# Kernel tuning notes

Measured on AMD Instinct MI355X. Metric: run time of the kernel, lower is better.

Reference implementation:

```python
import jax, jax.numpy as jnp
import numpy as np
from jax import lax

IN_FEATURES = 1024
NUM_TAGS = 128
C = NUM_TAGS + 3          # CRF adds start/stop (+1 pad slot per original code)
START_IDX = C - 2
STOP_IDX = C - 1
NEG = -10000.0


def setup_inputs() -> dict:
    key = jax.random.key(0)
    k1, k2, k3, k4 = jax.random.split(key, 4)
    B, L = 64, 512
    x = jax.random.normal(k1, (B, L, IN_FEATURES), dtype=jnp.float32)
    mask = jnp.ones((B, L), dtype=jnp.float32)
    W = jax.random.normal(k2, (C, IN_FEATURES), dtype=jnp.float32) * (1.0 / np.sqrt(IN_FEATURES))
    b = jax.random.normal(k3, (C,), dtype=jnp.float32) * 0.01
    transitions = jax.random.normal(k4, (C, C), dtype=jnp.float32)
    # transitions[i, j] = score of transitioning FROM j TO i
    transitions = transitions.at[START_IDX, :].set(NEG)   # never transition into start
    transitions = transitions.at[:, STOP_IDX].set(NEG)    # never transition out of stop
    return {"x": x, "mask": mask, "W": W, "b": b, "transitions": transitions}


def reference(x, mask, W, b, transitions):
    """CRF forward: linear projection + Viterbi decode.
    Returns (best_score [B], best_paths [B, L])."""
    feats = jnp.einsum("bld,cd->blc", x, W) + b          # [B, L, C]
    B, L, Cn = feats.shape

    init_score = jnp.full((B, Cn), NEG, dtype=feats.dtype).at[:, START_IDX].set(0.0)

    def viterbi_step(score, inp):
        feat_t, mask_t = inp                              # [B, C], [B]
        # acc[b, i, j] = score[b, j] + transitions[i, j]
        acc = score[:, None, :] + transitions[None, :, :]  # [B, C, C]
        best = jnp.max(acc, axis=-1)                      # [B, C]
        bp = jnp.argmax(acc, axis=-1).astype(jnp.int32)   # [B, C]
        m = mask_t[:, None]
        new_score = (best + feat_t) * m + score * (1.0 - m)
        return new_score, bp

    final_score, bps = lax.scan(
        viterbi_step, init_score,
        (jnp.transpose(feats, (1, 0, 2)), mask.T))        # bps: [L, B, C]

    final_score = final_score + transitions[STOP_IDX]     # [B, C]
    best_score = jnp.max(final_score, axis=-1)            # [B]
    best_tag = jnp.argmax(final_score, axis=-1).astype(jnp.int32)  # [B]

    def backtrack(tag, bp_t):
        # tag: current tag at timestep t; bp_t: [B, C] backpointers at t
        prev = jnp.take_along_axis(bp_t, tag[:, None], axis=1)[:, 0]
        return prev, tag                                  # emit tag at timestep t

    _, path = lax.scan(backtrack, best_tag, bps, reverse=True)  # path: [L, B]
    best_paths = path.T                                   # [B, L]
    return best_score, best_paths
```

## Files before the change

### kernel.cpp

```cpp
#include <hip/hip_runtime.h>

#define BB 64
#define LL 512
#define DD 1024
#define CC 131
#define CP 132
#define START_I 129
#define STOP_I 130
#define NEGV -10000.0f

__device__ __forceinline__ void lds_barrier() {
    asm volatile("s_waitcnt lgkmcnt(0)" ::: "memory");
    __builtin_amdgcn_s_barrier();
    __builtin_amdgcn_sched_barrier(0);
}

#define GM 64
#define GK 32
#define LSTR 36

__global__ __launch_bounds__(256, 2) void gemm_feats(
    const float* __restrict__ x, const float* __restrict__ W,
    const float* __restrict__ bias, float* __restrict__ feats)
{
    __shared__ float xs[GM * LSTR];
    __shared__ float ws[CP * LSTR];

    const int tid = threadIdx.x;
    const int m0 = blockIdx.x * GM;
    const int tm = tid & 15;
    const int tj = (tid >> 4) & 15;
    const bool tail = (tj < 3);
    const int tjt = (tj < 3) ? tj : 2;

    float acc[4][8];
    float acct[4];
#pragma unroll
    for (int r = 0; r < 4; ++r) {
        acct[r] = 0.f;
#pragma unroll
        for (int c = 0; c < 8; ++c) acc[r][c] = 0.f;
    }

    for (int kc = 0; kc < DD / GK; ++kc) {
        const int k0 = kc * GK;
        if (kc) __syncthreads();
#pragma unroll
        for (int q = 0; q < 2; ++q) {
            int lin = tid + q * 256;
            int m = lin >> 3, c4 = lin & 7;
            float4 v = *(const float4*)&x[(size_t)(m0 + m) * DD + k0 + c4 * 4];
            *(float4*)&xs[m * LSTR + c4 * 4] = v;
        }
#pragma unroll
        for (int q = 0; q < 5; ++q) {
            int lin = tid + q * 256;
            if (lin < CC * 8) {
                int r = lin >> 3, c4 = lin & 7;
                float4 v = *(const float4*)&W[(size_t)r * DD + k0 + c4 * 4];
                *(float4*)&ws[r * LSTR + c4 * 4] = v;
            }
        }
        __syncthreads();

#pragma unroll
        for (int k4 = 0; k4 < 8; ++k4) {
            float4 xr[4], wr[8], wt;
#pragma unroll
            for (int r = 0; r < 4; ++r)
                xr[r] = *(const float4*)&xs[(tm + 16 * r) * LSTR + k4 * 4];
#pragma unroll
            for (int c = 0; c < 8; ++c)
                wr[c] = *(const float4*)&ws[(tj + 16 * c) * LSTR + k4 * 4];
            wt = *(const float4*)&ws[(128 + tjt) * LSTR + k4 * 4];
#pragma unroll
            for (int r = 0; r < 4; ++r) {
#pragma unroll
                for (int c = 0; c < 8; ++c) {
                    acc[r][c] = fmaf(xr[r].x, wr[c].x, acc[r][c]);
                    acc[r][c] = fmaf(xr[r].y, wr[c].y, acc[r][c]);
                    acc[r][c] = fmaf(xr[r].z, wr[c].z, acc[r][c]);
                    acc[r][c] = fmaf(xr[r].w, wr[c].w, acc[r][c]);
                }
                acct[r] = fmaf(xr[r].x, wt.x, acct[r]);
                acct[r] = fmaf(xr[r].y, wt.y, acct[r]);
                acct[r] = fmaf(xr[r].z, wt.z, acct[r]);
                acct[r] = fmaf(xr[r].w, wt.w, acct[r]);
            }
        }
    }

#pragma unroll
    for (int c = 0; c < 8; ++c) {
        int j = tj + 16 * c;
        float bv = bias[j];
#pragma unroll
        for (int r = 0; r < 4; ++r)
            feats[(size_t)(m0 + tm + 16 * r) * CP + j] = acc[r][c] + bv;
    }
    if (tail) {
        int j = 128 + tj;
        float bv = bias[j];
#pragma unroll
        for (int r = 0; r < 4; ++r)
            feats[(size_t)(m0 + tm + 16 * r) * CP + j] = acct[r] + bv;
    }
}

__global__ __launch_bounds__(512, 1) void viterbi_fwd(
    const float* __restrict__ feats, const float* __restrict__ mask,
    const float* __restrict__ trans, float* __restrict__ hist)
{
    const int b = blockIdx.x;
    const int tid = threadIdx.x;
    const int w = tid >> 6, lane = tid & 63;

    __shared__ float sbuf[2][144];
    __shared__ float pbuf[7][132];

    const float* fb = feats + (size_t)b * LL * CP;
    const float* mb = mask + (size_t)b * LL;
    float* hb = hist + (size_t)b * LL * CP;

    int sub, trow = 0;
    bool twr = false;
    float4 TA[5], TB[5];
    if (w < 7) {
        sub = w;
        const int i0 = sub * 20;
        const float* trA = trans + (size_t)lane * CC;
        const float* trB = trans + (size_t)(64 + lane) * CC;
#pragma unroll
        for (int q = 0; q < 5; ++q) {
            int i = i0 + 4 * q;
            TA[q].x = (i + 0 < CC) ? trA[i + 0] : NEGV;
            TA[q].y = (i + 1 < CC) ? trA[i + 1] : NEGV;
            TA[q].z = (i + 2 < CC) ? trA[i + 2] : NEGV;
            TA[q].w = (i + 3 < CC) ? trA[i + 3] : NEGV;
            TB[q].x = (i + 0 < CC) ? trB[i + 0] : NEGV;
            TB[q].y = (i + 1 < CC) ? trB[i + 1] : NEGV;
            TB[q].z = (i + 2 < CC) ? trB[i + 2] : NEGV;
            TB[q].w = (i + 3 < CC) ? trB[i + 3] : NEGV;
        }
    } else {
        const int ln = (lane < 21) ? lane : 20;
        const int s7 = ln / 3;
        const int r3 = ln - s7 * 3;
        sub = s7;
        trow = 128 + r3;
        twr = (lane < 21);
        const int i0 = sub * 20;
        const float* tr = trans + (size_t)trow * CC;
#pragma unroll
        for (int q = 0; q < 5; ++q) {
            int i = i0 + 4 * q;
            TA[q].x = (i + 0 < CC) ? tr[i + 0] : NEGV;
            TA[q].y = (i + 1 < CC) ? tr[i + 1] : NEGV;
            TA[q].z = (i + 2 < CC) ? tr[i + 2] : NEGV;
            TA[q].w = (i + 3 < CC) ? tr[i + 3] : NEGV;
        }
    }

    for (int q = tid; q < 2 * 144; q += 512) {
        int bi = q / 144, idx = q - bi * 144;
        sbuf[bi][idx] = (bi == 0 && idx == START_I) ? 0.f : NEGV;
    }
    __syncthreads();

    const int k = tid;
    const bool cl = (tid < 131);
    float s_prev = (k == START_I) ? 0.f : NEGV;
    float fv0 = 0.f, fv1 = 0.f, mv0 = 1.f, mv1 = 1.f;
    if (cl) { fv0 = fb[k]; fv1 = fb[CP + k]; mv0 = mb[0]; mv1 = mb[1]; }
    const float* fb_t = fb + 2 * CP + k;
    const float* mb_t = mb + 2;
    float* hb_t = hb + k;

    for (int t = 0; t < LL; ++t) {
        const int rb = t & 1;

        {
            const float4* s4 = (const float4*)(&sbuf[rb][0]) + sub * 5;
            if (w < 7) {
                float a0 = -3.0e38f, a1 = -3.0e38f, b0 = -3.0e38f, b1 = -3.0e38f;
#pragma unroll
                for (int q = 0; q < 5; ++q) {
                    float4 sv = s4[q];
                    a0 = fmaxf(fmaxf(sv.x + TA[q].x, sv.y + TA[q].y), a0);
                    a1 = fmaxf(fmaxf(sv.z + TA[q].z, sv.w + TA[q].w), a1);
                    b0 = fmaxf(fmaxf(sv.x + TB[q].x, sv.y + TB[q].y), b0);
                    b1 = fmaxf(fmaxf(sv.z + TB[q].z, sv.w + TB[q].w), b1);
                }
                pbuf[sub][lane] = fmaxf(a0, a1);
                pbuf[sub][64 + lane] = fmaxf(b0, b1);
            } else {
                float a0 = -3.0e38f, a1 = -3.0e38f;
#pragma unroll
                for (int q = 0; q < 5; ++q) {
                    float4 sv = s4[q];
                    a0 = fmaxf(fmaxf(sv.x + TA[q].x, sv.y + TA[q].y), a0);
                    a1 = fmaxf(fmaxf(sv.z + TA[q].z, sv.w + TA[q].w), a1);
                }
                if (twr) pbuf[sub][trow] = fmaxf(a0, a1);
            }
        }

        lds_barrier();

        float fv2 = 0.f, mv2 = 1.f;
        if (cl && t + 2 < LL) { fv2 = *fb_t; mv2 = *mb_t; }
        fb_t += CP; ++mb_t;

        if (cl) {
            float p = fmaxf(fmaxf(fmaxf(pbuf[0][k], pbuf[1][k]),
                                  fmaxf(pbuf[2][k], pbuf[3][k])),
                            fmaxf(fmaxf(pbuf[4][k], pbuf[5][k]), pbuf[6][k]));
            float ns = (mv0 != 0.f) ? (p + fv0) : s_prev;
            s_prev = ns;
            sbuf[rb ^ 1][k] = ns;
            *hb_t = ns;
        }
        hb_t += CP;

        lds_barrier();

        fv0 = fv1; fv1 = fv2; mv0 = mv1; mv1 = mv2;
    }
}

__global__ __launch_bounds__(256, 4) void bp_kernel(
    const float* __restrict__ hist, const float* __restrict__ trans,
    unsigned char* __restrict__ bp)
{
    const int b  = blockIdx.x / 5;
    const int jc = blockIdx.x % 5;
    const int tc = blockIdx.y;
    const int tid = threadIdx.x;
    const int j0 = jc * 32;

    __shared__ float Ts[32][136];
    __shared__ float hs[8][132];

    for (int q = 0; q < 17; ++q) {
        int lin = tid + q * 256;
        if (lin < 32 * CC) {
            int r = lin / CC, i = lin - r * CC;
            if (j0 + r < CC) Ts[r][i] = trans[(size_t)(j0 + r) * CC + i];
        }
    }
    {
        const float4* src = (const float4*)(hist + ((size_t)b * LL + tc * 8) * CP);
#pragma unroll
        for (int q = 0; q < 2; ++q) {
            int lin = tid + q * 256;
            if (lin < (8 * CP) / 4) ((float4*)hs)[lin] = src[lin];
        }
    }
    __syncthreads();

    const int jl = tid & 31;
    const int tt = tid >> 5;
    const int j = j0 + jl;
    const int t = tc * 8 + tt + 1;
    if (j >= CC || t >= LL) return;

    float best; int idx;
    {
        float4 tv = *(const float4*)&Ts[jl][128];
        float4 hv = *(const float4*)&hs[tt][128];
        best = hv.z + tv.z; idx = 130;
        float v;
        v = hv.y + tv.y; if (v >= best) { best = v; idx = 129; }
        v = hv.x + tv.x; if (v >= best) { best = v; idx = 128; }
    }
#pragma unroll
    for (int i4 = 31; i4 >= 0; --i4) {
        float4 tv = *(const float4*)&Ts[jl][i4 * 4];
        float4 hv = *(const float4*)&hs[tt][i4 * 4];
        float v;
        v = hv.w + tv.w; if (v >= best) { best = v; idx = i4 * 4 + 3; }
        v = hv.z + tv.z; if (v >= best) { best = v; idx = i4 * 4 + 2; }
        v = hv.y + tv.y; if (v >= best) { best = v; idx = i4 * 4 + 1; }
        v = hv.x + tv.x; if (v >= best) { best = v; idx = i4 * 4 + 0; }
    }
    bp[((size_t)b * LL + t) * CP + j] = (unsigned char)idx;
}

__global__ __launch_bounds__(64, 1) void viterbi_btr(
    const float* __restrict__ hist, const float* __restrict__ trans,
    const unsigned char* __restrict__ bp,
    float* __restrict__ out_score, float* __restrict__ out_path)
{
    const int b = blockIdx.x;
    const int lane = threadIdx.x;
    const float* hb = hist + ((size_t)b * LL + (LL - 1)) * CP;
    const float* ts = trans + (size_t)STOP_I * CC;

    float v0 = hb[lane] + ts[lane];
    float v1 = hb[lane + 64] + ts[lane + 64];
    float v2 = (lane < 3) ? (hb[lane + 128] + ts[lane + 128]) : -3.0e38f;

    float best = v0; int idx = lane;
    if (v1 > best) { best = v1; idx = lane + 64; }
    if (v2 > best) { best = v2; idx = lane + 128; }
#pragma unroll
    for (int off = 32; off >= 1; off >>= 1) {
        float ob = __shfl_xor(best, off, 64);
        int   oi = __shfl_xor(idx, off, 64);
        if (ob > best || (ob == best && oi < idx)) { best = ob; idx = oi; }
    }

    float* op = out_path + (size_t)b * LL;
    if (lane == 0) {
        out_score[b] = best;
        op[LL - 1] = (float)idx;
    }
    int tag = idx;

    __shared__ unsigned char buf[2][1088];
    const unsigned char* bpb = bp + (size_t)b * LL * CP;

    {
        const unsigned int* src = (const unsigned int*)(bpb + (size_t)504 * CP);
        unsigned int* dst = (unsigned int*)buf[1];
#pragma unroll
        for (int q = 0; q < 5; ++q) {
            int lin = lane + q * 64;
            if (lin < 264) dst[lin] = src[lin];
        }
    }
    lds_barrier();

    int cur = 1;
    for (int k = 63; k >= 0; --k) {
        unsigned int r0 = 0, r1 = 0, r2 = 0, r3 = 0, r4 = 0;
        if (k > 0) {
            const unsigned int* src = (const unsigned int*)(bpb + (size_t)(k - 1) * 8 * CP);
            r0 = src[lane];
            r1 = src[lane + 64];
            r2 = src[lane + 128];
            r3 = src[lane + 192];
            if (lane < 8) r4 = src[lane + 256];
        }
        const unsigned char* cb = buf[cur];
#pragma unroll
        for (int s = 7; s >= 0; --s) {
            int t = k * 8 + s;
            if (t >= 1) {
                tag = cb[s * CP + tag];
                if (lane == 0) op[t - 1] = (float)tag;
            }
        }
        if (k > 0) {
            unsigned int* dst = (unsigned int*)buf[cur ^ 1];
            dst[lane] = r0;
            dst[lane + 64] = r1;
            dst[lane + 128] = r2;
            dst[lane + 192] = r3;
            if (lane < 8) dst[lane + 256] = r4;
            lds_barrier();
        }
        cur ^= 1;
    }
}

extern "C" void kernel_launch(void* const* d_in, const int* in_sizes, int n_in,
                              void* d_out, int out_size, void* d_ws, size_t ws_size,
                              hipStream_t stream)
{
    const float* x     = (const float*)d_in[0];
    const float* mask  = (const float*)d_in[1];
    const float* W     = (const float*)d_in[2];
    const float* bias  = (const float*)d_in[3];
    const float* trans = (const float*)d_in[4];

    float* feats = (float*)d_ws;
    float* hist  = feats + (size_t)BB * LL * CP;
    unsigned char* bp = (unsigned char*)(hist + (size_t)BB * LL * CP);
    float* out_score = (float*)d_out;
    float* out_path  = out_score + BB;

    hipLaunchKernelGGL(gemm_feats, dim3((BB * LL) / GM), dim3(256), 0, stream, x, W, bias, feats);
    hipLaunchKernelGGL(viterbi_fwd, dim3(BB), dim3(512), 0, stream, feats, mask, trans, hist);
    hipLaunchKernelGGL(bp_kernel, dim3(BB * 5, 64), dim3(256), 0, stream, hist, trans, bp);
    hipLaunchKernelGGL(viterbi_btr, dim3(BB), dim3(64), 0, stream, hist, trans, bp, out_score, out_path);
}
```

Baseline: 595.1 us.

## Enlarge GEMM per-thread tile and repartition Viterbi max-reduction across nine waves

The GEMM kernel now runs 128 threads per block, each computing an 8x8 output tile plus tail columns instead of 4x8, which raises register reuse but lowers the number of threads per block. The Viterbi forward kernel now splits the 128 main source columns into eight 16-wide chunks across eight waves. A ninth wave handles the destination rows 128-130. Each destination thread folds in the last three source columns (128-130) directly from shared memory, using its own transition values held in registers. This removes the padded uneven 20-wide chunks and the boundary checks in the serial per-step loop, but adds extra shared loads per step and a larger block.

```diff
diff --git a/kernel.cpp b/kernel.cpp
--- a/kernel.cpp
+++ b/kernel.cpp
@@ -19,7 +19,7 @@
 #define GK 32
 #define LSTR 36
 
-__global__ __launch_bounds__(256, 2) void gemm_feats(
+__global__ __launch_bounds__(128, 1) void gemm_feats(
     const float* __restrict__ x, const float* __restrict__ W,
     const float* __restrict__ bias, float* __restrict__ feats)
 {
@@ -28,15 +28,15 @@
 
     const int tid = threadIdx.x;
     const int m0 = blockIdx.x * GM;
-    const int tm = tid & 15;
-    const int tj = (tid >> 4) & 15;
+    const int tm = tid & 7;
+    const int tj = tid >> 3;
     const bool tail = (tj < 3);
     const int tjt = (tj < 3) ? tj : 2;
 
-    float acc[4][8];
-    float acct[4];
-#pragma unroll
-    for (int r = 0; r < 4; ++r) {
+    float acc[8][8];
+    float acct[8];
+#pragma unroll
+    for (int r = 0; r < 8; ++r) {
         acct[r] = 0.f;
 #pragma unroll
         for (int c = 0; c < 8; ++c) acc[r][c] = 0.f;
@@ -46,15 +46,15 @@
         const int k0 = kc * GK;
         if (kc) __syncthreads();
 #pragma unroll
-        for (int q = 0; q < 2; ++q) {
-            int lin = tid + q * 256;
+        for (int q = 0; q < 4; ++q) {
+            int lin = tid + q * 128;
             int m = lin >> 3, c4 = lin & 7;
             float4 v = *(const float4*)&x[(size_t)(m0 + m) * DD + k0 + c4 * 4];
             *(float4*)&xs[m * LSTR + c4 * 4] = v;
         }
 #pragma unroll
-        for (int q = 0; q < 5; ++q) {
-            int lin = tid + q * 256;
+        for (int q = 0; q < 9; ++q) {
+            int lin = tid + q * 128;
             if (lin < CC * 8) {
                 int r = lin >> 3, c4 = lin & 7;
                 float4 v = *(const float4*)&W[(size_t)r * DD + k0 + c4 * 4];
@@ -65,16 +65,16 @@
 
 #pragma unroll
         for (int k4 = 0; k4 < 8; ++k4) {
-            float4 xr[4], wr[8], wt;
-#pragma unroll
-            for (int r = 0; r < 4; ++r)
-                xr[r] = *(const float4*)&xs[(tm + 16 * r) * LSTR + k4 * 4];
+            float4 xr[8], wr[8], wt;
+#pragma unroll
+            for (int r = 0; r < 8; ++r)
+                xr[r] = *(const float4*)&xs[(tm + 8 * r) * LSTR + k4 * 4];
 #pragma unroll
             for (int c = 0; c < 8; ++c)
                 wr[c] = *(const float4*)&ws[(tj + 16 * c) * LSTR + k4 * 4];
             wt = *(const float4*)&ws[(128 + tjt) * LSTR + k4 * 4];
 #pragma unroll
-            for (int r = 0; r < 4; ++r) {
+            for (int r = 0; r < 8; ++r) {
 #pragma unroll
                 for (int c = 0; c < 8; ++c) {
                     acc[r][c] = fmaf(xr[r].x, wr[c].x, acc[r][c]);
@@ -95,19 +95,19 @@
         int j = tj + 16 * c;
         float bv = bias[j];
 #pragma unroll
-        for (int r = 0; r < 4; ++r)
-            feats[(size_t)(m0 + tm + 16 * r) * CP + j] = acc[r][c] + bv;
+        for (int r = 0; r < 8; ++r)
+            feats[(size_t)(m0 + tm + 8 * r) * CP + j] = acc[r][c] + bv;
     }
     if (tail) {
         int j = 128 + tj;
         float bv = bias[j];
 #pragma unroll
-        for (int r = 0; r < 4; ++r)
-            feats[(size_t)(m0 + tm + 16 * r) * CP + j] = acct[r] + bv;
-    }
-}
-
-__global__ __launch_bounds__(512, 1) void viterbi_fwd(
+        for (int r = 0; r < 8; ++r)
+            feats[(size_t)(m0 + tm + 8 * r) * CP + j] = acct[r] + bv;
+    }
+}
+
+__global__ __launch_bounds__(576, 1) void viterbi_fwd(
     const float* __restrict__ feats, const float* __restrict__ mask,
     const float* __restrict__ trans, float* __restrict__ hist)
 {
@@ -115,60 +115,56 @@
     const int tid = threadIdx.x;
     const int w = tid >> 6, lane = tid & 63;
 
-    __shared__ float sbuf[2][144];
-    __shared__ float pbuf[7][132];
+    __shared__ float sbuf[2][132];
+    __shared__ float pbuf[8][132];
 
     const float* fb = feats + (size_t)b * LL * CP;
     const float* mb = mask + (size_t)b * LL;
     float* hb = hist + (size_t)b * LL * CP;
 
-    int sub, trow = 0;
+    int sub, tcol = 0;
     bool twr = false;
-    float4 TA[5], TB[5];
-    if (w < 7) {
+    float4 TA[4], TB[4];
+    if (w < 8) {
         sub = w;
-        const int i0 = sub * 20;
-        const float* trA = trans + (size_t)lane * CC;
-        const float* trB = trans + (size_t)(64 + lane) * CC;
-#pragma unroll
-        for (int q = 0; q < 5; ++q) {
-            int i = i0 + 4 * q;
-            TA[q].x = (i + 0 < CC) ? trA[i + 0] : NEGV;
-            TA[q].y = (i + 1 < CC) ? trA[i + 1] : NEGV;
-            TA[q].z = (i + 2 < CC) ? trA[i + 2] : NEGV;
-            TA[q].w = (i + 3 < CC) ? trA[i + 3] : NEGV;
-            TB[q].x = (i + 0 < CC) ? trB[i + 0] : NEGV;
-            TB[q].y = (i + 1 < CC) ? trB[i + 1] : NEGV;
-            TB[q].z = (i + 2 < CC) ? trB[i + 2] : NEGV;
-            TB[q].w = (i + 3 < CC) ? trB[i + 3] : NEGV;
+        const float* trA = trans + (size_t)lane * CC + sub * 16;
+        const float* trB = trans + (size_t)(64 + lane) * CC + sub * 16;
+#pragma unroll
+        for (int q = 0; q < 4; ++q) {
+            TA[q].x = trA[4 * q + 0]; TA[q].y = trA[4 * q + 1];
+            TA[q].z = trA[4 * q + 2]; TA[q].w = trA[4 * q + 3];
+            TB[q].x = trB[4 * q + 0]; TB[q].y = trB[4 * q + 1];
+            TB[q].z = trB[4 * q + 2]; TB[q].w = trB[4 * q + 3];
         }
     } else {
-        const int ln = (lane < 21) ? lane : 20;
-        const int s7 = ln / 3;
-        const int r3 = ln - s7 * 3;
-        sub = s7;
-        trow = 128 + r3;
-        twr = (lane < 21);
-        const int i0 = sub * 20;
-        const float* tr = trans + (size_t)trow * CC;
-#pragma unroll
-        for (int q = 0; q < 5; ++q) {
-            int i = i0 + 4 * q;
-            TA[q].x = (i + 0 < CC) ? tr[i + 0] : NEGV;
-            TA[q].y = (i + 1 < CC) ? tr[i + 1] : NEGV;
-            TA[q].z = (i + 2 < CC) ? tr[i + 2] : NEGV;
-            TA[q].w = (i + 3 < CC) ? tr[i + 3] : NEGV;
-        }
-    }
-
-    for (int q = tid; q < 2 * 144; q += 512) {
-        int bi = q / 144, idx = q - bi * 144;
-        sbuf[bi][idx] = (bi == 0 && idx == START_I) ? 0.f : NEGV;
-    }
-    __syncthreads();
+        const int ln = (lane < 24) ? lane : 23;
+        sub = ln / 3;
+        tcol = 128 + (ln - sub * 3);
+        twr = (lane < 24);
+        const float* tr = trans + (size_t)tcol * CC + sub * 16;
+#pragma unroll
+        for (int q = 0; q < 4; ++q) {
+            TA[q].x = tr[4 * q + 0]; TA[q].y = tr[4 * q + 1];
+            TA[q].z = tr[4 * q + 2]; TA[q].w = tr[4 * q + 3];
+            TB[q] = TA[q];
+        }
+    }
 
     const int k = tid;
     const bool cl = (tid < 131);
+    float Tt0 = NEGV, Tt1 = NEGV, Tt2 = NEGV;
+    if (cl) {
+        Tt0 = trans[(size_t)k * CC + 128];
+        Tt1 = trans[(size_t)k * CC + 129];
+        Tt2 = trans[(size_t)k * CC + 130];
+    }
+
+    for (int q = tid; q < 2 * 132; q += 576) {
+        int bi = q / 132, idx = q - bi * 132;
+        sbuf[bi][idx] = (bi == 0 && idx == START_I) ? 0.f : NEGV;
+    }
+    __syncthreads();
+
     float s_prev = (k == START_I) ? 0.f : NEGV;
     float fv0 = 0.f, fv1 = 0.f, mv0 = 1.f, mv1 = 1.f;
     if (cl) { fv0 = fb[k]; fv1 = fb[CP + k]; mv0 = mb[0]; mv1 = mb[1]; }
@@ -180,11 +176,11 @@
         const int rb = t & 1;
 
         {
-            const float4* s4 = (const float4*)(&sbuf[rb][0]) + sub * 5;
-            if (w < 7) {
+            const float4* s4 = (const float4*)(&sbuf[rb][0]) + sub * 4;
+            if (w < 8) {
                 float a0 = -3.0e38f, a1 = -3.0e38f, b0 = -3.0e38f, b1 = -3.0e38f;
 #pragma unroll
-                for (int q = 0; q < 5; ++q) {
+                for (int q = 0; q < 4; ++q) {
                     float4 sv = s4[q];
                     a0 = fmaxf(fmaxf(sv.x + TA[q].x, sv.y + TA[q].y), a0);
                     a1 = fmaxf(fmaxf(sv.z + TA[q].z, sv.w + TA[q].w), a1);
@@ -196,12 +192,12 @@
             } else {
                 float a0 = -3.0e38f, a1 = -3.0e38f;
 #pragma unroll
-                for (int q = 0; q < 5; ++q) {
+                for (int q = 0; q < 4; ++q) {
                     float4 sv = s4[q];
                     a0 = fmaxf(fmaxf(sv.x + TA[q].x, sv.y + TA[q].y), a0);
                     a1 = fmaxf(fmaxf(sv.z + TA[q].z, sv.w + TA[q].w), a1);
                 }
-                if (twr) pbuf[sub][trow] = fmaxf(a0, a1);
+                if (twr) pbuf[sub][tcol] = fmaxf(a0, a1);
             }
         }
 
@@ -214,7 +210,10 @@
         if (cl) {
             float p = fmaxf(fmaxf(fmaxf(pbuf[0][k], pbuf[1][k]),
                                   fmaxf(pbuf[2][k], pbuf[3][k])),
-                            fmaxf(fmaxf(pbuf[4][k], pbuf[5][k]), pbuf[6][k]));
+                            fmaxf(fmaxf(pbuf[4][k], pbuf[5][k]),
+                                  fmaxf(pbuf[6][k], pbuf[7][k])));
+            float s128 = sbuf[rb][128], s129 = sbuf[rb][129], s130 = sbuf[rb][130];
+            p = fmaxf(p, fmaxf(fmaxf(s128 + Tt0, s129 + Tt1), s130 + Tt2));
             float ns = (mv0 != 0.f) ? (p + fv0) : s_prev;
             s_prev = ns;
             sbuf[rb ^ 1][k] = ns;
@@ -380,8 +379,8 @@
     float* out_score = (float*)d_out;
     float* out_path  = out_score + BB;
 
-    hipLaunchKernelGGL(gemm_feats, dim3((BB * LL) / GM), dim3(256), 0, stream, x, W, bias, feats);
-    hipLaunchKernelGGL(viterbi_fwd, dim3(BB), dim3(512), 0, stream, feats, mask, trans, hist);
+    hipLaunchKernelGGL(gemm_feats, dim3((BB * LL) / GM), dim3(128), 0, stream, x, W, bias, feats);
+    hipLaunchKernelGGL(viterbi_fwd, dim3(BB), dim3(576), 0, stream, feats, mask, trans, hist);
     hipLaunchKernelGGL(bp_kernel, dim3(BB * 5, 64), dim3(256), 0, stream, hist, trans, bp);
     hipLaunchKernelGGL(viterbi_btr, dim3(BB), dim3(64), 0, stream, hist, trans, bp, out_score, out_path);
 }
```

New measurement: 706.2 us. 1.19x slower.

## Double-buffer GEMM shared-memory tiles with register prefetch of next K chunk

Applied to the files above, without the earlier changes.

The projection GEMM now loads the next K-chunk of x and W from global memory into registers before computing on the current LDS buffer, then stores them into the alternate LDS buffer. This uses a single barrier per iteration instead of two. The aim is to hide global-load latency behind the FMA work. In exchange it doubles LDS use and adds prefetch registers, and the launch-bounds occupancy hint drops from 2 blocks per CU to unspecified, which may lower occupancy.

```diff
diff --git a/kernel.cpp b/kernel.cpp
--- a/kernel.cpp
+++ b/kernel.cpp
@@ -19,12 +19,12 @@
 #define GK 32
 #define LSTR 36
 
-__global__ __launch_bounds__(256, 2) void gemm_feats(
+__global__ __launch_bounds__(256) void gemm_feats(
     const float* __restrict__ x, const float* __restrict__ W,
     const float* __restrict__ bias, float* __restrict__ feats)
 {
-    __shared__ float xs[GM * LSTR];
-    __shared__ float ws[CP * LSTR];
+    __shared__ float xs[2][GM * LSTR];
+    __shared__ float ws[2][CP * LSTR];
 
     const int tid = threadIdx.x;
     const int m0 = blockIdx.x * GM;
@@ -33,6 +33,9 @@
     const bool tail = (tj < 3);
     const int tjt = (tj < 3) ? tj : 2;
 
+    const int xm = tid >> 3, xc4 = tid & 7;
+    const int w0r = tid >> 3, w0c = tid & 7;
+
     float acc[4][8];
     float acct[4];
 #pragma unroll
@@ -42,37 +45,55 @@
         for (int c = 0; c < 8; ++c) acc[r][c] = 0.f;
     }
 
+    float4 px[2], pw[5];
+
+#define LOADK(KC)                                                                 \
+    {                                                                             \
+        const int k0 = (KC) * GK;                                                 \
+        px[0] = *(const float4*)&x[(size_t)(m0 + xm) * DD + k0 + xc4 * 4];        \
+        px[1] = *(const float4*)&x[(size_t)(m0 + xm + 32) * DD + k0 + xc4 * 4];   \
+        _Pragma("unroll")                                                         \
+        for (int q = 0; q < 5; ++q) {                                             \
+            int lin = tid + q * 256;                                              \
+            if (lin < CC * 8) {                                                   \
+                int r = lin >> 3, c4 = lin & 7;                                   \
+                pw[q] = *(const float4*)&W[(size_t)r * DD + k0 + c4 * 4];         \
+            }                                                                     \
+        }                                                                         \
+    }
+
+#define STOREK(BUF)                                                               \
+    {                                                                             \
+        *(float4*)&xs[BUF][xm * LSTR + xc4 * 4] = px[0];                          \
+        *(float4*)&xs[BUF][(xm + 32) * LSTR + xc4 * 4] = px[1];                   \
+        _Pragma("unroll")                                                         \
+        for (int q = 0; q < 5; ++q) {                                             \
+            int lin = tid + q * 256;                                              \
+            if (lin < CC * 8) {                                                   \
+                int r = lin >> 3, c4 = lin & 7;                                   \
+                *(float4*)&ws[BUF][r * LSTR + c4 * 4] = pw[q];                    \
+            }                                                                     \
+        }                                                                         \
+    }
+
+    LOADK(0)
+    STOREK(0)
+    __syncthreads();
+
     for (int kc = 0; kc < DD / GK; ++kc) {
-        const int k0 = kc * GK;
-        if (kc) __syncthreads();
-#pragma unroll
-        for (int q = 0; q < 2; ++q) {
-            int lin = tid + q * 256;
-            int m = lin >> 3, c4 = lin & 7;
-            float4 v = *(const float4*)&x[(size_t)(m0 + m) * DD + k0 + c4 * 4];
-            *(float4*)&xs[m * LSTR + c4 * 4] = v;
-        }
-#pragma unroll
-        for (int q = 0; q < 5; ++q) {
-            int lin = tid + q * 256;
-            if (lin < CC * 8) {
-                int r = lin >> 3, c4 = lin & 7;
-                float4 v = *(const float4*)&W[(size_t)r * DD + k0 + c4 * 4];
-                *(float4*)&ws[r * LSTR + c4 * 4] = v;
-            }
-        }
-        __syncthreads();
+        const int cur = kc & 1;
+        if (kc + 1 < DD / GK) LOADK(kc + 1)
 
 #pragma unroll
         for (int k4 = 0; k4 < 8; ++k4) {
             float4 xr[4], wr[8], wt;
 #pragma unroll
             for (int r = 0; r < 4; ++r)
-                xr[r] = *(const float4*)&xs[(tm + 16 * r) * LSTR + k4 * 4];
+                xr[r] = *(const float4*)&xs[cur][(tm + 16 * r) * LSTR + k4 * 4];
 #pragma unroll
             for (int c = 0; c < 8; ++c)
-                wr[c] = *(const float4*)&ws[(tj + 16 * c) * LSTR + k4 * 4];
-            wt = *(const float4*)&ws[(128 + tjt) * LSTR + k4 * 4];
+                wr[c] = *(const float4*)&ws[cur][(tj + 16 * c) * LSTR + k4 * 4];
+            wt = *(const float4*)&ws[cur][(128 + tjt) * LSTR + k4 * 4];
 #pragma unroll
             for (int r = 0; r < 4; ++r) {
 #pragma unroll
@@ -88,7 +109,14 @@
                 acct[r] = fmaf(xr[r].w, wt.w, acct[r]);
             }
         }
-    }
+
+        if (kc + 1 < DD / GK) {
+            STOREK(cur ^ 1)
+            lds_barrier();
+        }
+    }
+#undef LOADK
+#undef STOREK
 
 #pragma unroll
     for (int c = 0; c < 8; ++c) {
```

Measured after the change: 786.9 us. 32.2% more time.
